# Optimization experiments

Measured on AMD Instinct MI355X. Metric: run time of the kernel, lower is better.

The kernel has to match this reference:

```python
import jax, jax.numpy as jnp
import numpy as np
from jax import lax

KERNEL_SIZES = (3, 5, 7)
EPS = 1e-12  # torch F.normalize default eps


def _gamma(x, k):
    """SpatialCorrelationSampler(kernel_size=k)(x, F.normalize(x, dim=1)).

    With patch_size=1, stride=1, padding=0, dilation=1 the sampler output at
    (b, y, x) is sum over channels and the kxk window of in1 * in2. Since
    in2 = in1 / max(||in1||_c, eps), the channel contraction collapses to
    ||x||^2 / max(||x||, eps) per pixel, followed by a kxk box-sum (VALID).
    x: [B, C, H, W] -> gamma: [B, H-k+1, W-k+1]
    """
    norm = jnp.sqrt(jnp.sum(x * x, axis=1))          # [B, H, W]
    p = (norm * norm) / jnp.maximum(norm, EPS)       # [B, H, W]
    return lax.reduce_window(p, 0.0, lax.add, (1, k, k), (1, 1, 1), 'VALID')


def reference(out_feat0, out_feat1, gt_feat0, gt_feat1):
    loss = jnp.float32(0.0)
    for xo, xg in ((out_feat0, gt_feat0), (out_feat1, gt_feat1)):
        for k in KERNEL_SIZES:
            go = _gamma(xo, k)
            gg = _gamma(xg, k)
            loss = loss + jnp.mean((go - gg) ** 2)   # nn.MSELoss (mean)
    return loss


def setup_inputs() -> dict:
    key = jax.random.key(0)
    k0, k1, k2, k3 = jax.random.split(key, 4)
    return {
        'out_feat0': jax.random.normal(k0, (8, 256, 64, 64), dtype=jnp.float32),
        'out_feat1': jax.random.normal(k1, (8, 512, 32, 32), dtype=jnp.float32),
        'gt_feat0': jax.random.normal(k2, (8, 256, 64, 64), dtype=jnp.float32),
        'gt_feat1': jax.random.normal(k3, (8, 512, 32, 32), dtype=jnp.float32),
    }
```

## Files before the change

kernel.cpp:

```cpp
#include <hip/hip_runtime.h>
#include <math.h>

#define EPS 1e-12f

typedef float f4 __attribute__((ext_vector_type(4)));

template <int W, int C, int H>
__device__ __forceinline__ void row_kernel(
    const float* __restrict__ xo, const float* __restrict__ xg,
    float* __restrict__ r,
    int bh, int tid, float* lds , float* drow )
{
    constexpr int QUADS  = W / 4;
    constexpr int CCHUNK = 256 / QUADS;
    constexpr int CPT    = C / CCHUNK;
    constexpr int NR     = 8 * H;

    const int quad = tid % QUADS;
    const int cgrp = tid / QUADS;
    const int b    = bh / H;
    const int h    = bh % H;

    const int plane = H * W;
    const int base  = b * C * plane + h * W + quad * 4;
    const int c0    = cgrp * CPT;

    f4 so = {0.f, 0.f, 0.f, 0.f};
    f4 sg = {0.f, 0.f, 0.f, 0.f};
#pragma unroll 4
    for (int i = 0; i < CPT; ++i) {
        const int off = base + (c0 + i) * plane;
        const f4 vo = __builtin_nontemporal_load(reinterpret_cast<const f4*>(xo + off));
        const f4 vg = __builtin_nontemporal_load(reinterpret_cast<const f4*>(xg + off));
        so += vo * vo;
        sg += vg * vg;
    }

    *reinterpret_cast<f4*>(lds + (0 * CCHUNK + cgrp) * W + quad * 4) = so;
    *reinterpret_cast<f4*>(lds + (1 * CCHUNK + cgrp) * W + quad * 4) = sg;
    __syncthreads();

    if (tid < W) {
        float ao = 0.f, ag = 0.f;
#pragma unroll
        for (int g = 0; g < CCHUNK; ++g) {
            ao += lds[(0 * CCHUNK + g) * W + tid];
            ag += lds[(1 * CCHUNK + g) * W + tid];
        }
        const float no = sqrtf(ao);
        const float ng = sqrtf(ag);
        const float po = ao / fmaxf(no, EPS);
        const float pg = ag / fmaxf(ng, EPS);
        drow[tid] = po - pg;
    }
    __syncthreads();

#pragma unroll
    for (int ki = 0; ki < 3; ++ki) {
        const int k = 3 + 2 * ki;
        const int V = W - k + 1;
        if (tid < V) {
            float s = 0.f;
#pragma unroll
            for (int j = 0; j < 7; ++j)
                if (j < k) s += drow[tid + j];
            r[(ki * NR + bh) * W + tid] = s;
        }
    }
}

__global__ __launch_bounds__(256) void stage1_kernel(
    const float* __restrict__ o0, const float* __restrict__ g0,
    const float* __restrict__ o1, const float* __restrict__ g1,
    float* __restrict__ r0, float* __restrict__ r1,
    float* __restrict__ out)
{
    __shared__ float lds[2048];
    __shared__ float drow[64];
    const int bid = blockIdx.x;
    if (bid == 0 && threadIdx.x == 0) out[0] = 0.0f;
    if (bid < 8 * 64) {
        row_kernel<64, 256, 64>(o0, g0, r0, bid, threadIdx.x, lds, drow);
    } else {
        row_kernel<32, 512, 32>(o1, g1, r1, bid - 8 * 64, threadIdx.x, lds, drow);
    }
}

__global__ __launch_bounds__(256) void boxmse_kernel(
    const float* __restrict__ r0, const float* __restrict__ r1,
    float* __restrict__ out)
{
    __shared__ float img[64 * 62];
    __shared__ float wsum[4];

    const int bid = blockIdx.x;
    const int t   = bid / 24;
    const int rem = bid % 24;
    const int b   = rem / 3;
    const int ki  = rem % 3;
    const int k   = 3 + 2 * ki;
    const int H   = (t == 0) ? 64 : 32;
    const int V   = H - k + 1;
    const float* src = ((t == 0) ? r0 : r1) + (ki * (8 * H) + b * H) * H;

    const int tid = threadIdx.x;

    for (int i = tid; i < H * V; i += 256) {
        const int y = i / V;
        const int x = i - y * V;
        img[i] = src[y * H + x];
    }
    __syncthreads();

    float acc = 0.f;
    for (int i = tid; i < V * V; i += 256) {
        const int y = i / V;
        const int x = i - y * V;
        float s = 0.f;
        for (int j = 0; j < k; ++j) s += img[(y + j) * V + x];
        acc = fmaf(s, s, acc);
    }

    for (int off = 32; off > 0; off >>= 1) acc += __shfl_down(acc, off);
    if ((tid & 63) == 0) wsum[tid >> 6] = acc;
    __syncthreads();
    if (tid == 0) {
        const float total = wsum[0] + wsum[1] + wsum[2] + wsum[3];
        const float inv_count = 1.0f / (float)(8 * V * V);
        atomicAdd(out, total * inv_count);
    }
}

extern "C" void kernel_launch(void* const* d_in, const int* in_sizes, int n_in,
                              void* d_out, int out_size, void* d_ws, size_t ws_size,
                              hipStream_t stream) {
    const float* out_feat0 = (const float*)d_in[0];
    const float* out_feat1 = (const float*)d_in[1];
    const float* gt_feat0  = (const float*)d_in[2];
    const float* gt_feat1  = (const float*)d_in[3];
    float* out = (float*)d_out;

    float* r0 = (float*)d_ws;
    float* r1 = r0 + 3 * 512 * 64;

    stage1_kernel<<<8 * 64 + 8 * 32, 256, 0, stream>>>(
        out_feat0, gt_feat0, out_feat1, gt_feat1, r0, r1, out);
    boxmse_kernel<<<48, 256, 0, stream>>>(r0, r1, out);
}
```

Before: 128.7 us.

## Fuse row stage and box-MSE stage into one cooperative kernel with grid sync

Merges the two kernels into a single cooperative launch of 768 blocks that synchronise with a grid-wide barrier before the first 48 blocks run the box-sum MSE phase. The aim is to remove the second kernel launch and the gap between dependent launches. In exchange it adds cooperative launch overhead and a grid barrier, and every block must be co-resident. The launch-bounds hint of 3 blocks per CU is set so that 768 blocks can fit at once.

Measured after the change: 340.9 us. +164.8%, slower.

```diff
diff --git a/kernel.cpp b/kernel.cpp
--- a/kernel.cpp
+++ b/kernel.cpp
@@ -1,12 +1,15 @@
 #include <hip/hip_runtime.h>
+#include <hip/hip_cooperative_groups.h>
 #include <math.h>
+
+namespace cg = cooperative_groups;
 
 #define EPS 1e-12f
 
 typedef float f4 __attribute__((ext_vector_type(4)));
 
 template <int W, int C, int H>
-__device__ __forceinline__ void row_kernel(
+__device__ __forceinline__ void row_phase(
     const float* __restrict__ xo, const float* __restrict__ xg,
     float* __restrict__ r,
     int bh, int tid, float* lds , float* drow )
@@ -69,31 +72,37 @@
     }
 }
 
-__global__ __launch_bounds__(256) void stage1_kernel(
+__global__ __launch_bounds__(256, 3) void fused_kernel(
     const float* __restrict__ o0, const float* __restrict__ g0,
     const float* __restrict__ o1, const float* __restrict__ g1,
     float* __restrict__ r0, float* __restrict__ r1,
     float* __restrict__ out)
 {
-    __shared__ float lds[2048];
-    __shared__ float drow[64];
-    const int bid = blockIdx.x;
-    if (bid == 0 && threadIdx.x == 0) out[0] = 0.0f;
-    if (bid < 8 * 64) {
-        row_kernel<64, 256, 64>(o0, g0, r0, bid, threadIdx.x, lds, drow);
-    } else {
-        row_kernel<32, 512, 32>(o1, g1, r1, bid - 8 * 64, threadIdx.x, lds, drow);
-    }
-}
-
-__global__ __launch_bounds__(256) void boxmse_kernel(
-    const float* __restrict__ r0, const float* __restrict__ r1,
-    float* __restrict__ out)
-{
-    __shared__ float img[64 * 62];
-    __shared__ float wsum[4];
+    __shared__ float smem[64 * 62 + 4];
 
     const int bid = blockIdx.x;
+    const int tid = threadIdx.x;
+
+    if (bid == 0 && tid == 0) out[0] = 0.0f;
+    {
+        float* lds  = smem;
+        float* drow = smem + 2048;
+        if (bid < 8 * 64) {
+            row_phase<64, 256, 64>(o0, g0, r0, bid, tid, lds, drow);
+        } else {
+            row_phase<32, 512, 32>(o1, g1, r1, bid - 8 * 64, tid, lds, drow);
+        }
+    }
+
+    __threadfence();
+    cg::this_grid().sync();
+
+    if (bid >= 48) return;
+
+    float* img  = smem;
+    float* wsum = smem + 64 * 62;
+    __syncthreads();
+
     const int t   = bid / 24;
     const int rem = bid % 24;
     const int b   = rem / 3;
@@ -102,8 +111,6 @@
     const int H   = (t == 0) ? 64 : 32;
     const int V   = H - k + 1;
     const float* src = ((t == 0) ? r0 : r1) + (ki * (8 * H) + b * H) * H;
-
-    const int tid = threadIdx.x;
 
     for (int i = tid; i < H * V; i += 256) {
         const int y = i / V;
@@ -143,7 +150,12 @@
     float* r0 = (float*)d_ws;
     float* r1 = r0 + 3 * 512 * 64;
 
-    stage1_kernel<<<8 * 64 + 8 * 32, 256, 0, stream>>>(
-        out_feat0, gt_feat0, out_feat1, gt_feat1, r0, r1, out);
-    boxmse_kernel<<<48, 256, 0, stream>>>(r0, r1, out);
+    void* args[] = {
+        (void*)&out_feat0, (void*)&gt_feat0,
+        (void*)&out_feat1, (void*)&gt_feat1,
+        (void*)&r0, (void*)&r1, (void*)&out,
+    };
+    hipLaunchCooperativeKernel((const void*)fused_kernel,
+                               dim3(8 * 64 + 8 * 32), dim3(256),
+                               args, 0, stream);
 }
```
